# Kernel optimization log

Measured on AMD Instinct MI355X. Metric: run time of the kernel, lower is better.

Reference implementation:

```python
import jax, jax.numpy as jnp
import numpy as np

MAX_LEVEL = 3
FULL_LEN = 2 ** MAX_LEVEL  # wavelet_full_len for db1, mode='zero'


def _make_patterns():
    # Per-feature input to the DWT is [v, 0, ..., 0] (scalar zero-padded to 2**j).
    # Haar/db1 'zero' DWT of that signal is v times a fixed sparse pattern:
    # cA (len 1) = v*2^(-j/2); cD_k first element = v*2^(-k/2), rest zeros.
    pats = []
    for j in range(1, MAX_LEVEL + 1):
        vec = [2.0 ** (-j / 2.0)]                      # cA, length 1
        for k in range(1, j + 1):                      # cD_1 .. cD_j
            seg = np.zeros(2 ** (j - k))
            seg[0] = 2.0 ** (-k / 2.0)
            vec.extend(seg.tolist())
        full = np.zeros(FULL_LEN, dtype=np.float32)
        arr = np.asarray(vec, dtype=np.float32)
        full[: arr.shape[0]] = arr                     # F.pad to wavelet_full_len
        pats.append(full)
    return jnp.asarray(np.stack(pats))                 # (MAX_LEVEL, FULL_LEN)

_P = _make_patterns()


def _gumbel_hard(logits, gumb):
    # F.gumbel_softmax(logits, tau=1.0, hard=True), one sample per feature row.
    y = jax.nn.softmax(logits[None, :] + gumb, axis=-1)          # (feat, L)
    hard = jax.nn.one_hot(jnp.argmax(y, axis=-1), y.shape[-1], dtype=y.dtype)
    return jax.lax.stop_gradient(hard - y) + y                   # straight-through


def _wavelet_layer(x, logits, gumb, Wnl, bnl, Wwo, bwo):
    # Collapses the per-feature/per-level torch double loop:
    # xi_wave(level j) = v * (Wnl[f] . P[j]) + bnl[f]
    a = Wnl @ _P.T                       # (feat, levels)
    w = _gumbel_hard(logits, gumb)       # (feat, levels), one-hot rows
    coeff = jnp.sum(w * a, axis=-1)      # (feat,)
    agg = x * coeff + bnl                # (B, N, feat)
    return agg @ Wwo + bwo               # linear_out


def _mix(h, res_proj):
    diff = jnp.mean((h - res_proj) ** 2)
    th = jax.nn.sigmoid(diff)
    return th * h + (1.0 - th) * res_proj


def reference(x, adj, Wres, bres,
              Wg0, bg0, Wrg0, brg0, logits0, gumb0, Wnl0, bnl0, Wwo0, bwo0, Wrw0, brw0,
              Wg1, bg1, Wrg1, brg1, logits1, gumb1, Wnl1, bnl1, Wwo1, bwo1, Wrw1, brw1):
    res = x @ Wres + bres                                        # (B,N,Dout)
    # ---- layer 0 ----
    xg = jnp.einsum('ij,bjf->bif', adj, x) @ Wg0 + bg0           # 64->256: no residual add
    xg = _mix(xg, res @ Wrg0 + brg0)
    xw = _wavelet_layer(xg, logits0, gumb0, Wnl0, bnl0, Wwo0, bwo0) + xg  # 256==256: add
    xw = _mix(xw, res @ Wrw0 + brw0)
    # ---- layer 1 ----
    xg1 = jnp.einsum('ij,bjf->bif', adj, xw) @ Wg1 + bg1 + xw    # 256==256: add
    xg1 = _mix(xg1, res @ Wrg1 + brg1)
    xw1 = _wavelet_layer(xg1, logits1, gumb1, Wnl1, bnl1, Wwo1, bwo1)     # 256->64: no add
    xw1 = _mix(xw1, res @ Wrw1 + brw1)
    return xw1


def setup_inputs() -> dict:
    key = jax.random.key(0)
    ks = jax.random.split(key, 32)
    B, N, D_in, H, D_out = 128, 512, 64, 256, 64
    s = 0.05
    inp = {
        'x': jax.random.normal(ks[0], (B, N, D_in), jnp.float32),
        'adj': jax.random.uniform(ks[1], (N, N), jnp.float32) / N,
        'Wres': jax.random.normal(ks[2], (D_in, D_out), jnp.float32) * s,
        'bres': jax.random.normal(ks[3], (D_out,), jnp.float32) * s,
        'Wg0': jax.random.normal(ks[4], (D_in, H), jnp.float32) * s,
        'bg0': jax.random.normal(ks[5], (H,), jnp.float32) * s,
        'Wrg0': jax.random.normal(ks[6], (D_out, H), jnp.float32) * s,
        'brg0': jax.random.normal(ks[7], (H,), jnp.float32) * s,
        'logits0': jax.random.normal(ks[8], (3,), jnp.float32),
        'gumb0': jax.random.gumbel(ks[9], (H, 3), jnp.float32),
        'Wnl0': jax.random.normal(ks[10], (H, FULL_LEN), jnp.float32) * s,
        'bnl0': jax.random.normal(ks[11], (H,), jnp.float32) * s,
        'Wwo0': jax.random.normal(ks[12], (H, H), jnp.float32) * s,
        'bwo0': jax.random.normal(ks[13], (H,), jnp.float32) * s,
        'Wrw0': jax.random.normal(ks[14], (D_out, H), jnp.float32) * s,
        'brw0': jax.random.normal(ks[15], (H,), jnp.float32) * s,
        'Wg1': jax.random.normal(ks[16], (H, H), jnp.float32) * s,
        'bg1': jax.random.normal(ks[17], (H,), jnp.float32) * s,
        'Wrg1': jax.random.normal(ks[18], (D_out, H), jnp.float32) * s,
        'brg1': jax.random.normal(ks[19], (H,), jnp.float32) * s,
        'logits1': jax.random.normal(ks[20], (3,), jnp.float32),
        'gumb1': jax.random.gumbel(ks[21], (H, 3), jnp.float32),
        'Wnl1': jax.random.normal(ks[22], (H, FULL_LEN), jnp.float32) * s,
        'bnl1': jax.random.normal(ks[23], (H,), jnp.float32) * s,
        'Wwo1': jax.random.normal(ks[24], (H, D_out), jnp.float32) * s,
        'bwo1': jax.random.normal(ks[25], (D_out,), jnp.float32) * s,
        'Wrw1': jax.random.normal(ks[26], (D_out, D_out), jnp.float32) * s,
        'brw1': jax.random.normal(ks[27], (D_out,), jnp.float32) * s,
    }
    return inp
```

## Files before the change

kernel.cpp:

```cpp
#include <hip/hip_runtime.h>
#include <hip/hip_bf16.h>
#include <math.h>

#define BB   128
#define NN   512
#define DIN  64
#define HH   256
#define DOUT 64
#define BNR  (BB * NN)

typedef float  f32x4  __attribute__((ext_vector_type(4)));
typedef __bf16 bf16x8 __attribute__((ext_vector_type(8)));

#define GLP(p)  ((const __attribute__((address_space(1))) void*)(p))
#define LDSP(p) ((__attribute__((address_space(3))) void*)(p))

__constant__ float PAT[3][8] = {
    {0.70710678f, 0.70710678f, 0.f, 0.f, 0.f, 0.f, 0.f, 0.f},
    {0.5f,        0.70710678f, 0.f, 0.5f, 0.f, 0.f, 0.f, 0.f},
    {0.35355339f, 0.70710678f, 0.f, 0.f, 0.f, 0.5f, 0.f, 0.35355339f}
};

__device__ __forceinline__ unsigned short f2bfu(float x) {
    __hip_bfloat16 b = __float2bfloat16(x);
// ... 37 lines not shown
    __syncthreads();
    #pragma unroll
    for (int j = 0; j < FN; ++j) {
        int colb = (wn * (FN * 16) + j * 16 + lc) * 2;
        #pragma unroll
        for (int i = 0; i < FM; ++i) {
            int row0 = wm * (FM * 16) + i * 16 + lr4;
            #pragma unroll
            for (int r = 0; r < 4; ++r) {
                int row = row0 + r;
                *reinterpret_cast<unsigned short*>(
                    lds + row * (BN * 2) + (colb ^ (((row >> 2) & 3) << 5))) =
                    f2bfu(a[i][j][r]);
            }
        }
    }
    __syncthreads();
    const int TPR = BN / 8;
    const int RPP = 256 / TPR;
    #pragma unroll
    for (int p = 0; p < BM / RPP; ++p) {
        int row = p * RPP + tid / TPR;
        int cb = (tid % TPR) * 16;
        int pb = cb ^ (((row >> 2) & 3) << 5);
        uint4 v = *reinterpret_cast<const uint4*>(lds + row * (BN * 2) + pb);
        *reinterpret_cast<uint4*>(reinterpret_cast<char*>(C + base + (long)row * N) + cb) = v;
    }
}

template<int BM, int BN, int FM, int FN>
__device__ __forceinline__ void write_tileT(char* lds, f32x4 (&a)[FM][FN],
                                            __hip_bfloat16* __restrict__ CT,
                                            long baseT, int ldT, int tid)
{
    const int wave = tid >> 6;
    const int lane = tid & 63;
    const int wm = wave >> 1, wn = wave & 1;
    const int lc = lane & 15;
    const int lr4 = (lane >> 4) << 2;
    __syncthreads();
    #pragma unroll
    for (int j = 0; j < FN; ++j) {
        int c = wn * (FN * 16) + j * 16 + lc;
        int cbase = c * (BM * 2);
        int swz = ((c >> 2) & 3) << 5;
        #pragma unroll
        for (int i = 0; i < FM; ++i) {
            int m0 = wm * (FM * 16) + i * 16 + lr4;
            #pragma unroll
            for (int r = 0; r < 4; ++r) {
                int m = m0 + r;
                *reinterpret_cast<unsigned short*>(lds + cbase + ((m * 2) ^ swz)) =
                    f2bfu(a[i][j][r]);
            }
        }
    }
    __syncthreads();
    const int TPR = BM / 8;
    const int RPP = 256 / TPR;
    #pragma unroll
    for (int p = 0; p < BN / RPP; ++p) {
        int c = p * RPP + tid / TPR;
        int tb = (tid % TPR) * 16;
        int pb = tb ^ (((c >> 2) & 3) << 5);
        uint4 v = *reinterpret_cast<const uint4*>(lds + c * (BM * 2) + pb);
        *reinterpret_cast<uint4*>(reinterpret_cast<char*>(CT + baseT + (long)c * ldT) + tb) = v;
    }
}

template<int BM, int BN>
__device__ __forceinline__ void stage_tiles(const __hip_bfloat16* __restrict__ Ab,
                                            const __hip_bfloat16* __restrict__ Bb,
                                            char* AsB, char* BsB,
                                            int m0, int n0, int k0, int KA, int KB,
                                            int wave, int lane)
{
    const int NCH = (BM + BN) / 32;
    const int lr = lane >> 3;
    const int ls = lane & 7;
    #pragma unroll
    for (int cc = 0; cc < NCH; ++cc) {
        int c = wave * NCH + cc;
        const __hip_bfloat16* src;
        char* ldsb;
        if (c < BM / 8) {
            int r = c * 8 + lr;
            ldsb = AsB + c * 1024;
            src = Ab + ((long)(m0 + r) * KA + k0 + ((ls ^ (r & 7)) << 3));
        } else {
            int c2 = c - BM / 8;
            int r = c2 * 8 + lr;
            ldsb = BsB + c2 * 1024;
            src = Bb + ((long)(n0 + r) * KB + k0 + ((ls ^ (r & 7)) << 3));
        }
        __builtin_amdgcn_global_load_lds(GLP(src), LDSP(ldsb), 16, 0, 0);
    }
}

template<int BM, int BN, int FM, int FN>
__device__ __forceinline__ void mfma_tiles(char* AsB, char* BsB,
                                           f32x4 (&acc)[FM][FN], int wave, int lane)
{
    const int wm = wave >> 1, wn = wave & 1;
    #pragma unroll
    for (int ksl = 0; ksl < 2; ++ksl) {
        bf16x8 af[FM], bfr[FN];
        #pragma unroll
        for (int i = 0; i < FM; ++i) {
            int row = wm * (FM * 16) + i * 16 + (lane & 15);
            int off = (ksl * 64 + ((lane >> 4) << 4)) ^ ((row & 7) << 4);
            af[i] = *reinterpret_cast<const bf16x8*>(AsB + row * 128 + off);
        }
        #pragma unroll
        for (int j = 0; j < FN; ++j) {
            int row = wn * (FN * 16) + j * 16 + (lane & 15);
            int off = (ksl * 64 + ((lane >> 4) << 4)) ^ ((row & 7) << 4);
            bfr[j] = *reinterpret_cast<const bf16x8*>(BsB + row * 128 + off);
        }
        #pragma unroll
        for (int i = 0; i < FM; ++i)
            #pragma unroll
            for (int j = 0; j < FN; ++j)
                acc[i][j] = __builtin_amdgcn_mfma_f32_16x16x32_bf16(
                    af[i], bfr[j], acc[i][j], 0, 0, 0);
    }
}

template<int BM, int BN, int FM, int FN, int NS, int NA>
__device__ __forceinline__ void pipe_run(
    const __hip_bfloat16* const (&sA)[NS], const __hip_bfloat16* const (&sB)[NS],
    const int (&sK)[NS], const int (&sk0)[NS],
    char* buf0, char* buf1,
    f32x4 (&acc0)[FM][FN], f32x4 (&acc1)[FM][FN],
    int m0, int n0, int wave, int lane)
{
    constexpr int BOFF = BM * 128;
    stage_tiles<BM, BN>(sA[0], sB[0], buf0, buf0 + BOFF, m0, n0, sk0[0],
                        sK[0], sK[0], wave, lane);
    __syncthreads();
    #pragma unroll
    for (int t = 0; t < NS; ++t) {
        char* bc = (t & 1) ? buf1 : buf0;
        if (t + 1 < NS) {
            char* bn = (t & 1) ? buf0 : buf1;
            stage_tiles<BM, BN>(sA[t + 1], sB[t + 1], bn, bn + BOFF, m0, n0,
                                sk0[t + 1], sK[t + 1], sK[t + 1], wave, lane);
        }
        if (t < NA) mfma_tiles<BM, BN, FM, FN>(bc, bc + BOFF, acc0, wave, lane);
        else        mfma_tiles<BM, BN, FM, FN>(bc, bc + BOFF, acc1, wave, lane);
        __syncthreads();
    }
}

__global__ __launch_bounds__(256) void cvta_k(const float* __restrict__ adj,
                                              unsigned int* __restrict__ adjb,
                                              float* __restrict__ ars)
{
    int n = blockIdx.x;
    int t = threadIdx.x;
    float2 v = reinterpret_cast<const float2*>(adj)[n * 256 + t];
    adjb[n * 256 + t] = (unsigned int)f2bfu(v.x) | ((unsigned int)f2bfu(v.y) << 16);
    __shared__ float sm[256];
    sm[t] = v.x + v.y;
    __syncthreads();
    for (int o = 128; o > 0; o >>= 1) {
        if (t < o) sm[t] += sm[t + o];
        __syncthreads();
    }
    if (t == 0) ars[n] = sm[0];
}

__global__ __launch_bounds__(256) void cvtx_k(const float* __restrict__ in,
                                              unsigned short* __restrict__ rm,
                                              unsigned short* __restrict__ tr)
{
    __shared__ float t[64][65];
    const long base = (long)blockIdx.z * NN * DIN;
    const int r0 = blockIdx.y * 64;
    const int tr4 = threadIdx.x >> 6;
    const int tc  = threadIdx.x & 63;
    #pragma unroll
    for (int i = 0; i < 16; ++i) {
        int r = i * 4 + tr4;
        float v = in[base + (long)(r0 + r) * DIN + tc];
        t[r][tc] = v;
        rm[base + (long)(r0 + r) * DIN + tc] = f2bfu(v);
    }
    __syncthreads();
    #pragma unroll
    for (int i = 0; i < 16; ++i) {
        int d = i * 4 + tr4;
        tr[base + (long)d * NN + r0 + tc] = f2bfu(t[tc][d]);
    }
}

__device__ __forceinline__ void tcvt_body(const float* __restrict__ in,
                                          unsigned short* __restrict__ out,
                                          const float* __restrict__ cs, float us,
                                          int R, int C, int r0, int c0)
{
    __shared__ float t[64][65];
    int tr = threadIdx.x >> 6;
    int tc = threadIdx.x & 63;
    #pragma unroll
    for (int i = 0; i < 16; ++i) {
        int r = i * 4 + tr;
        t[r][tc] = in[(long)(r0 + r) * C + c0 + tc];
    }
    __syncthreads();
    float sc = (cs ? cs[r0 + tc] : 1.0f) * us;
    #pragma unroll
    for (int i = 0; i < 16; ++i) {
        int r = i * 4 + tr;
        out[(long)(c0 + r) * R + r0 + tc] = f2bfu(t[tc][r] * sc);
    }
}

struct WTArgs {
    const float* src[8];
    unsigned short* dst[8];
    const float* cs[8];
    float sgn[8];
    int R[8], C[8];
};
__global__ __launch_bounds__(256) void tcvt_w_k(WTArgs a)
{
    int wgt = blockIdx.y;
    int R = a.R[wgt], C = a.C[wgt];
    int tilesX = C >> 6;
    int tiles = (R >> 6) * tilesX;
    int t = blockIdx.x;
    if (t >= tiles) return;
    tcvt_body(a.src[wgt], a.dst[wgt], a.cs[wgt], a.sgn[wgt], R, C,
              (t / tilesX) * 64, (t % tilesX) * 64);
}

__global__ void coeff2_k(const float* __restrict__ logits0, const float* __restrict__ gumb0,
                         const float* __restrict__ Wnl0, float* __restrict__ c0,
                         const float* __restrict__ logits1, const float* __restrict__ gumb1,
                         const float* __restrict__ Wnl1, float* __restrict__ c1)
{
    const float* lg = blockIdx.x ? logits1 : logits0;
    const float* gb = blockIdx.x ? gumb1 : gumb0;
    const float* Wn = blockIdx.x ? Wnl1 : Wnl0;
    float* cc = blockIdx.x ? c1 : c0;
    int f = threadIdx.x;
    float l0 = lg[0] + gb[f * 3 + 0];
    float l1 = lg[1] + gb[f * 3 + 1];
    float l2 = lg[2] + gb[f * 3 + 2];
    int bl = 0;
    float bv = l0;
    if (l1 > bv) { bv = l1; bl = 1; }
    if (l2 > bv) { bv = l2; bl = 2; }
    float s = 0.f;
    #pragma unroll
    for (int t = 0; t < 8; ++t) s += Wn[f * 8 + t] * PAT[bl][t];
    cc[f] = s;
}

struct FVArgs {
    const float* W[6];
    const float* c[6];
    const float* v[6];
    const float* base[6];
    float* out[6];
    int K[6], N[6];
};
__global__ __launch_bounds__(256) void foldvec_k(FVArgs a)
{
    int cs = blockIdx.y;
    int n = blockIdx.x;
    if (n >= a.N[cs]) return;
    int k = threadIdx.x;
    float s = 0.f;
    if (k < a.K[cs]) {
        float cc = a.c[cs] ? a.c[cs][k] : 1.0f;
        s = a.v[cs][k] * cc * a.W[cs][(long)k * a.N[cs] + n];
    }
    __shared__ float sm[256];
    sm[threadIdx.x] = s;
    __syncthreads();
    for (int o = 128; o > 0; o >>= 1) {
        if (threadIdx.x < o) sm[threadIdx.x] += sm[threadIdx.x + o];
        __syncthreads();
    }
    if (threadIdx.x == 0)
        a.out[cs][n] = (a.base[cs] ? a.base[cs][n] : 0.f) + sm[0];
}

struct WFArgs {
    const float* Wsrc[4];
    const float* Wbig[4];
    const float* c[4];
    int incl[4], N[4];
    unsigned short* dst[4];
};
__global__ __launch_bounds__(256) void wfold_k(WFArgs a)
{
    int cs = blockIdx.y;
    int m = blockIdx.x;
    __shared__ float ws[256];
    const float* c = a.c[cs];
    ws[threadIdx.x] = a.Wsrc[cs][m * 256 + threadIdx.x] * (c ? c[threadIdx.x] : 1.0f);
    __syncthreads();
    int n = threadIdx.x;
    int N = a.N[cs];
    if (n >= N) return;
    float s = a.incl[cs] ? a.Wsrc[cs][m * 256 + n] : 0.f;
    const float* Wb = a.Wbig[cs];
    #pragma unroll 8
    for (int k = 0; k < 256; ++k)
        s += ws[k] * Wb[(long)k * N + n];
    a.dst[cs][n * 64 + m] = f2bfu(s);
}

__global__ __launch_bounds__(256) void sc0_k(
    const float* __restrict__ partial, int np, float inv_n,
    unsigned short* __restrict__ Wa,
    unsigned short* __restrict__ Wb,
    const float* __restrict__ bg0p, const float* __restrict__ brg0p,
    const float* __restrict__ crow0, float* __restrict__ cv0)
{
    __shared__ float red[256];
    float th = block_th(partial, np, inv_n, red, threadIdx.x);
    float om = 1.f - th;
    int g = blockIdx.x * 256 + threadIdx.x;
    Wa[g] = f2bfu(th * bf2f(Wa[g]));
    Wb[g] = f2bfu(om * bf2f(Wb[g]));
    if (g < 256) cv0[g] = th * bg0p[g] + om * brg0p[g] + crow0[g];
}

__global__ __launch_bounds__(256) void sc1_k(
    const float* __restrict__ partial, int np, float inv_n,
    unsigned short* __restrict__ Wg1T,
    const unsigned short* __restrict__ Wrw0T, const unsigned short* __restrict__ Wrg0pT,
    unsigned short* __restrict__ WcombT,
    unsigned short* __restrict__ Wg0pT,
    unsigned short* __restrict__ WrwWg1T,
    const float* __restrict__ bg1, const float* __restrict__ brw0,
    const float* __restrict__ cv0, const float* __restrict__ bw1v,
    float* __restrict__ bv1g, float* __restrict__ bw1s)
{
    __shared__ float red[256];
    float th = block_th(partial, np, inv_n, red, threadIdx.x);
    float om = 1.f - th;
    int g = blockIdx.x * 256 + threadIdx.x;
    Wg1T[g] = f2bfu(th * bf2f(Wg1T[g]));
    if (g < 16384) {
        WcombT[g]  = f2bfu(th * bf2f(Wrg0pT[g]) + om * bf2f(Wrw0T[g]));
        Wg0pT[g]   = f2bfu(th * bf2f(Wg0pT[g]));
        WrwWg1T[g] = f2bfu(om * bf2f(WrwWg1T[g]));
    }
    if (g < 256) {
        bv1g[g] = bg1[g] + om * brw0[g] + th * cv0[g];
        bw1s[g] = om * bw1v[g];
    }
}

__global__ __launch_bounds__(256) void sc2_k(
    const float* __restrict__ partial, int np, float inv_n,
    unsigned short* __restrict__ Wc1T,
    unsigned short* __restrict__ Wrgc1T,
    const float* __restrict__ brgc1, const float* __restrict__ crow1,
    float* __restrict__ cv2)
{
    __shared__ float red[256];
    float th = block_th(partial, np, inv_n, red, threadIdx.x);
    float om = 1.f - th;
    int g = blockIdx.x * 256 + threadIdx.x;
    Wc1T[g] = f2bfu(th * bf2f(Wc1T[g]));
    if (g < 4096) Wrgc1T[g] = f2bfu(om * bf2f(Wrgc1T[g]));
    if (g < 64) cv2[g] = om * brgc1[g] + crow1[g];
}

template<int BM, int BN, int FM, int FN>
__global__ __launch_bounds__(256) void gemm_res_k(
    const __hip_bfloat16* __restrict__ A, const __hip_bfloat16* __restrict__ Bt,
    const float* __restrict__ bias,
    __hip_bfloat16* __restrict__ Cb, __hip_bfloat16* __restrict__ CbT,
    int M, int N, int K)
{
    __shared__ __attribute__((aligned(128))) char lds[(BM + BN) * 128];
    char* AsB = lds;
    char* BsB = lds + BM * 128;

    const int m0 = blockIdx.y * BM;
    const int tid  = threadIdx.x;
    const int wave = tid >> 6;
    const int lane = tid & 63;
    const int wn = wave & 1;

    f32x4 acc[FM][FN];
    #pragma unroll
    for (int i = 0; i < FM; ++i)
        #pragma unroll
        for (int j = 0; j < FN; ++j)
            acc[i][j] = (f32x4){0.f, 0.f, 0.f, 0.f};

    for (int k0 = 0; k0 < K; k0 += 64) {
        stage_tiles<BM, BN>(A, Bt, AsB, BsB, m0, 0, k0, K, K, wave, lane);
        __syncthreads();
        mfma_tiles<BM, BN, FM, FN>(AsB, BsB, acc, wave, lane);
        __syncthreads();
    }

    const int lc = lane & 15;
    #pragma unroll
    for (int j = 0; j < FN; ++j) {
        float bv = bias[wn * (FN * 16) + j * 16 + lc];
        #pragma unroll
        for (int i = 0; i < FM; ++i)
            #pragma unroll
            for (int r = 0; r < 4; ++r)
                acc[i][j][r] += bv;
    }
    write_tile<BM, BN, FM, FN>(lds, acc, Cb, (long)m0 * N, N, tid);
    long baseT = (long)(m0 / NN) * ((long)N * NN) + (m0 % NN);
    write_tileT<BM, BN, FM, FN>(lds, acc, CbT, baseT, NN, tid);
}

template<int BM, int BN, int FM, int FN, int GX, int NB, int NS>
__global__ __launch_bounds__(256) void gemm_bt_swz_k(
    const __hip_bfloat16* __restrict__ A, const __hip_bfloat16* __restrict__ Bt,
    __hip_bfloat16* __restrict__ Cb,
    int M, int N, int K, long sA, long sB, long sC)
{
    __shared__ __attribute__((aligned(128))) char lds[2 * (BM + BN) * 128];

    const int d   = blockIdx.x;
    const int xcd = d & 7;
    const int q   = d >> 3;
    const int t   = q % NB;
    const int bz  = xcd + ((q / NB) << 3);
    const int n0  = (t % GX) * BN;
    const int m0  = (t / GX) * BM;

    const __hip_bfloat16* Ab = A + (long)bz * sA;
    const __hip_bfloat16* Bb = Bt + (long)bz * sB;

    const int tid  = threadIdx.x;
    const int wave = tid >> 6;
    const int lane = tid & 63;

    f32x4 acc[FM][FN];
    #pragma unroll
    for (int i = 0; i < FM; ++i)
        #pragma unroll
        for (int j = 0; j < FN; ++j)
            acc[i][j] = (f32x4){0.f, 0.f, 0.f, 0.f};

    const __hip_bfloat16* pA[NS];
    const __hip_bfloat16* pB[NS];
    int pK[NS], pk0[NS];
    #pragma unroll
    for (int s = 0; s < NS; ++s) { pA[s] = Ab; pB[s] = Bb; pK[s] = K; pk0[s] = s * 64; }

    pipe_run<BM, BN, FM, FN, NS, NS>(pA, pB, pK, pk0,
                                     lds, lds + (BM + BN) * 128,
                                     acc, acc, m0, n0, wave, lane);

    write_tile<BM, BN, FM, FN>(lds, acc, Cb, (long)bz * sC + (long)m0 * N + n0, N, tid);
}

template<int BM, int BN, int FM, int FN>
__global__ __launch_bounds__(256) void dual1_k(
    const __hip_bfloat16* __restrict__ A0, const __hip_bfloat16* __restrict__ B0, int K0,
    const __hip_bfloat16* __restrict__ A1, const __hip_bfloat16* __restrict__ B1, int K1,
    const float* __restrict__ b1, const float* __restrict__ b2,
    float* __restrict__ partial, int M, int N)
{
    __shared__ __attribute__((aligned(128))) char lds[2 * (BM + BN) * 128];

    const int d   = blockIdx.x;
    const int q   = d >> 3;
    const int nx  = q & 1;
    const int my  = (d & 7) + ((q >> 1) << 3);
    const int m0  = my * BM;
    const int n0  = nx * BN;

    const int tid  = threadIdx.x;
    const int wave = tid >> 6;
    const int lane = tid & 63;
    const int wn = wave & 1;

    f32x4 acc[FM][FN];
    #pragma unroll
    for (int i = 0; i < FM; ++i)
        #pragma unroll
        for (int j = 0; j < FN; ++j)
            acc[i][j] = (f32x4){0.f, 0.f, 0.f, 0.f};

    const __hip_bfloat16* pA[2] = {A0, A1};
    const __hip_bfloat16* pB[2] = {B0, B1};
    int pK[2] = {K0, K1};
    int pk0[2] = {0, 0};
    pipe_run<BM, BN, FM, FN, 2, 2>(pA, pB, pK, pk0,
                                   lds, lds + (BM + BN) * 128,
                                   acc, acc, m0, n0, wave, lane);

    const int lc = lane & 15;
    float dsum = 0.f;
    #pragma unroll
    for (int j = 0; j < FN; ++j) {
        int col = n0 + wn * (FN * 16) + j * 16 + lc;
        float bd = b1[col] - b2[col];
        #pragma unroll
        for (int i = 0; i < FM; ++i)
            #pragma unroll
            for (int r = 0; r < 4; ++r) {
                float dd = acc[i][j][r] + bd;
                dsum += dd * dd;
            }
    }

    float* red = (float*)lds;
    red[tid] = dsum;
    __syncthreads();
    for (int o = 128; o > 0; o >>= 1) {
        if (tid < o) red[tid] += red[tid + o];
        __syncthreads();
    }
    if (tid == 0) partial[my * 2 + nx] = red[0];
}

template<int BM, int BN, int FM, int FN>
__global__ __launch_bounds__(256) void wave2T_k(
    const __hip_bfloat16* __restrict__ A0, const __hip_bfloat16* __restrict__ B0, int K0,
    const __hip_bfloat16* __restrict__ A1, const __hip_bfloat16* __restrict__ B1, int K1,
    const __hip_bfloat16* __restrict__ A2, const __hip_bfloat16* __restrict__ B2, int K2,
    const float* __restrict__ cv, const float* __restrict__ b2v,
    __hip_bfloat16* __restrict__ C1T, float* __restrict__ partial_out, int M, int N)
{
    __shared__ __attribute__((aligned(128))) char lds[2 * (BM + BN) * 128];

    const int d   = blockIdx.x;
    const int q   = d >> 3;
    const int nx  = q & 1;
    const int my  = (d & 7) + ((q >> 1) << 3);
    const int m0  = my * BM;
    const int n0  = nx * BN;

    const int tid  = threadIdx.x;
    const int wave = tid >> 6;
    const int lane = tid & 63;
    const int wn = wave & 1;

    f32x4 acc0[FM][FN], acc1[FM][FN];
    #pragma unroll
    for (int i = 0; i < FM; ++i)
        #pragma unroll
        for (int j = 0; j < FN; ++j) {
            acc0[i][j] = (f32x4){0.f, 0.f, 0.f, 0.f};
            acc1[i][j] = (f32x4){0.f, 0.f, 0.f, 0.f};
        }

    const __hip_bfloat16* pA[3] = {A0, A1, A2};
    const __hip_bfloat16* pB[3] = {B0, B1, B2};
    int pK[3] = {K0, K1, K2};
    int pk0[3] = {0, 0, 0};
    pipe_run<BM, BN, FM, FN, 3, 2>(pA, pB, pK, pk0,
                                   lds, lds + (BM + BN) * 128,
                                   acc0, acc1, m0, n0, wave, lane);

    const int lc = lane & 15;
    float dsum = 0.f;
    #pragma unroll
    for (int j = 0; j < FN; ++j) {
        int col = n0 + wn * (FN * 16) + j * 16 + lc;
        float c1 = cv[col];
        float c2 = b2v[col];
        #pragma unroll
// ... 132 lines not shown
    const __hip_bfloat16* pA[6] = {A0, A0, A0, A0, A1, A2};
    const __hip_bfloat16* pB[6] = {B0, B0, B0, B0, B1, B2};
    int pK[6]  = {K0, K0, K0, K0, K1, K2};
    int pk0[6] = {0, 64, 128, 192, 0, 0};
    pipe_run<BM, BN, FM, FN, 6, 5>(pA, pB, pK, pk0,
                                   lds, lds + (BM + BN) * 128,
                                   acc0, acc1, m0, n0, wave, lane);

    const int lc = lane & 15;
    float dsum = 0.f;
    #pragma unroll
    for (int j = 0; j < FN; ++j) {
        int col = n0 + wn * (FN * 16) + j * 16 + lc;
        float c1 = cv[col];
        float c2 = b2v[col];
        #pragma unroll
        for (int i = 0; i < FM; ++i)
            #pragma unroll
            for (int r = 0; r < 4; ++r) {
                float v1 = acc0[i][j][r] + c1;
                float v2 = acc1[i][j][r] + c2;
                acc0[i][j][r] = v1;
                acc1[i][j][r] = v2;
                float dd = v1 - v2;
                dsum += dd * dd;
            }
    }

    float* red = (float*)lds;
    red[tid] = dsum;
    __syncthreads();
    for (int o = 128; o > 0; o >>= 1) {
        if (tid < o) red[tid] += red[tid + o];
        __syncthreads();
    }
    if (tid == 0) partial_out[pidx] = red[0];

    write_tile<BM, BN, FM, FN>(lds, acc0, C1, (long)m0 * N + n0, N, tid);
    write_tile<BM, BN, FM, FN>(lds, acc1, C2, (long)m0 * N + n0, N, tid);
}

__global__ __launch_bounds__(256) void mixfinal_k(
    const unsigned short* __restrict__ h, const unsigned short* __restrict__ r,
    const float* __restrict__ partial_in, int np_in, float inv_in,
    float* __restrict__ out, long n4)
{
    __shared__ float sm[256];
    const float th = block_th(partial_in, np_in, inv_in, sm, (int)threadIdx.x);
    const float om = 1.f - th;
    long gid = (long)blockIdx.x * 256 + threadIdx.x;
    long stride = (long)gridDim.x * 256;
    for (long i = gid; i < n4; i += stride) {
        ushort4 hv = reinterpret_cast<const ushort4*>(h)[i];
        ushort4 rv = reinterpret_cast<const ushort4*>(r)[i];
        float4 o;
        o.x = th * bf2f(hv.x) + om * bf2f(rv.x);
        o.y = th * bf2f(hv.y) + om * bf2f(rv.y);
        o.z = th * bf2f(hv.z) + om * bf2f(rv.z);
        o.w = th * bf2f(hv.w) + om * bf2f(rv.w);
        reinterpret_cast<float4*>(out)[i] = o;
    }
}

extern "C" void kernel_launch(void* const* d_in, const int* in_sizes, int n_in,
                              void* d_out, int out_size, void* d_ws, size_t ws_size,
                              hipStream_t stream)
{
    const float* x       = (const float*)d_in[0];
    const float* adj     = (const float*)d_in[1];
    const float* Wres    = (const float*)d_in[2];
    const float* bres    = (const float*)d_in[3];
    const float* Wg0     = (const float*)d_in[4];
    const float* bg0     = (const float*)d_in[5];
    const float* Wrg0    = (const float*)d_in[6];
    const float* brg0    = (const float*)d_in[7];
    const float* logits0 = (const float*)d_in[8];
    const float* gumb0   = (const float*)d_in[9];
    const float* Wnl0    = (const float*)d_in[10];
    const float* bnl0    = (const float*)d_in[11];
    const float* Wwo0    = (const float*)d_in[12];
    const float* bwo0    = (const float*)d_in[13];
    const float* Wrw0    = (const float*)d_in[14];
    const float* brw0    = (const float*)d_in[15];
    const float* Wg1     = (const float*)d_in[16];
    const float* bg1     = (const float*)d_in[17];
    const float* Wrg1    = (const float*)d_in[18];
    const float* brg1    = (const float*)d_in[19];
    const float* logits1 = (const float*)d_in[20];
    const float* gumb1   = (const float*)d_in[21];
    const float* Wnl1    = (const float*)d_in[22];
    const float* bnl1    = (const float*)d_in[23];
    const float* Wwo1    = (const float*)d_in[24];
    const float* bwo1    = (const float*)d_in[25];
    const float* Wrw1    = (const float*)d_in[26];
    const float* brw1    = (const float*)d_in[27];

    float* out = (float*)d_out;

    char* w = (char*)d_ws;
    auto alloc = [&](long bytes) { char* p = w; w += (bytes + 255) & ~255L; return p; };
    const long SLOT = (long)BNR * HH * 2;
    char* pool = alloc(5 * SLOT);
    __hip_bfloat16* Rbf  = (__hip_bfloat16*)alloc((long)BNR * DOUT * 2);
    __hip_bfloat16* adjb = (__hip_bfloat16*)alloc((long)NN * NN * 2);
    __hip_bfloat16* WT   = (__hip_bfloat16*)alloc(225280L * 2);
    float* partial0 = (float*)alloc(2048 * 4);
    float* partial1 = (float*)alloc(2048 * 4);
    float* partial2 = (float*)alloc(2048 * 4);
    float* partial3 = (float*)alloc(2048 * 4);
    float* c0      = (float*)alloc(256 * 4);
    float* c1      = (float*)alloc(256 * 4);
    float* bg0p    = (float*)alloc(256 * 4);
    float* brg0p   = (float*)alloc(256 * 4);
    float* crow0   = (float*)alloc(256 * 4);
    float* brgc1   = (float*)alloc(64 * 4);
    float* crow1   = (float*)alloc(64 * 4);
    float* cv0     = (float*)alloc(256 * 4);
    float* bv1g    = (float*)alloc(256 * 4);
    float* cv2     = (float*)alloc(64 * 4);
    float* ars     = (float*)alloc(512 * 4);
    float* bw1v    = (float*)alloc(256 * 4);
    float* bw1s    = (float*)alloc(256 * 4);

    auto S = [&](int i) { return pool + (long)i * SLOT; };
    __hip_bfloat16* xwrT = (__hip_bfloat16*)S(0);
    __hip_bfloat16* orw  = (__hip_bfloat16*)S(1);
    __hip_bfloat16* rw1  = (__hip_bfloat16*)(S(1) + (long)BNR * DOUT * 2);
    __hip_bfloat16* Radj = (__hip_bfloat16*)(S(1) + 2L * BNR * DOUT * 2);
    __hip_bfloat16* xg1  = (__hip_bfloat16*)S(2);
    __hip_bfloat16* T1x  = (__hip_bfloat16*)S(3);
    __hip_bfloat16* xbf  = (__hip_bfloat16*)S(4);
    __hip_bfloat16* xT   = (__hip_bfloat16*)(S(4) + (long)BNR * DIN * 2);
    __hip_bfloat16* T0   = (__hip_bfloat16*)(S(4) + 2L * BNR * DIN * 2);
    __hip_bfloat16* RbfT = (__hip_bfloat16*)(S(4) + 3L * BNR * DIN * 2);

    __hip_bfloat16* WresT   = WT;
    __hip_bfloat16* Wg0T    = WT + 4096;
    __hip_bfloat16* Wrg0T   = WT + 20480;
    __hip_bfloat16* Wrw0T   = WT + 36864;
    __hip_bfloat16* Wg1T    = WT + 53248;
    __hip_bfloat16* Wrg1T   = WT + 118784;
    __hip_bfloat16* Wc1T    = WT + 135168;
    __hip_bfloat16* Wrw1T   = WT + 151552;
    __hip_bfloat16* Wg0pT   = WT + 155648;
    __hip_bfloat16* Wrg0pT  = WT + 172032;
    __hip_bfloat16* Wrgc1T  = WT + 188416;
    __hip_bfloat16* WcombT  = WT + 192512;
    __hip_bfloat16* WrwWg1T = WT + 208896;

    const dim3 blk(256);
    const float invH = 1.0f / ((float)BNR * HH);
    const float invD = 1.0f / ((float)BNR * DOUT);

    hipLaunchKernelGGL(coeff2_k, dim3(2), dim3(256), 0, stream,
                       logits0, gumb0, Wnl0, c0, logits1, gumb1, Wnl1, c1);
    hipLaunchKernelGGL(cvta_k, dim3(NN), blk, 0, stream, adj, (unsigned int*)adjb, ars);
    hipLaunchKernelGGL(cvtx_k, dim3(1, 8, BB), blk, 0, stream, x,
                       (unsigned short*)xbf, (unsigned short*)xT);

    WTArgs wa;
    wa.src[0] = Wres; wa.dst[0] = (unsigned short*)WresT; wa.cs[0] = nullptr; wa.sgn[0] = 1.f;  wa.R[0] = 64;  wa.C[0] = 64;
    wa.src[1] = Wg0;  wa.dst[1] = (unsigned short*)Wg0T;  wa.cs[1] = nullptr; wa.sgn[1] = 1.f;  wa.R[1] = 64;  wa.C[1] = 256;
    wa.src[2] = Wrg0; wa.dst[2] = (unsigned short*)Wrg0T; wa.cs[2] = nullptr; wa.sgn[2] = -1.f; wa.R[2] = 64;  wa.C[2] = 256;
    wa.src[3] = Wrw0; wa.dst[3] = (unsigned short*)Wrw0T; wa.cs[3] = nullptr; wa.sgn[3] = 1.f;  wa.R[3] = 64;  wa.C[3] = 256;
    wa.src[4] = Wg1;  wa.dst[4] = (unsigned short*)Wg1T;  wa.cs[4] = nullptr; wa.sgn[4] = 1.f;  wa.R[4] = 256; wa.C[4] = 256;
    wa.src[5] = Wrg1; wa.dst[5] = (unsigned short*)Wrg1T; wa.cs[5] = nullptr; wa.sgn[5] = 1.f;  wa.R[5] = 64;  wa.C[5] = 256;
    wa.src[6] = Wwo1; wa.dst[6] = (unsigned short*)Wc1T;  wa.cs[6] = c1;      wa.sgn[6] = 1.f;  wa.R[6] = 256; wa.C[6] = 64;
    wa.src[7] = Wrw1; wa.dst[7] = (unsigned short*)Wrw1T; wa.cs[7] = nullptr; wa.sgn[7] = 1.f;  wa.R[7] = 64;  wa.C[7] = 64;
    hipLaunchKernelGGL(tcvt_w_k, dim3(16, 8), blk, 0, stream, wa);

    WFArgs wf;
    wf.Wsrc[0] = Wg0;  wf.Wbig[0] = Wwo0; wf.c[0] = c0;      wf.incl[0] = 1; wf.N[0] = 256;
    wf.dst[0] = (unsigned short*)Wg0pT;
    wf.Wsrc[1] = Wrg0; wf.Wbig[1] = Wwo0; wf.c[1] = c0;      wf.incl[1] = 1; wf.N[1] = 256;
    wf.dst[1] = (unsigned short*)Wrg0pT;
    wf.Wsrc[2] = Wrg1; wf.Wbig[2] = Wwo1; wf.c[2] = c1;      wf.incl[2] = 0; wf.N[2] = 64;
    wf.dst[2] = (unsigned short*)Wrgc1T;
    wf.Wsrc[3] = Wrw0; wf.Wbig[3] = Wg1;  wf.c[3] = nullptr; wf.incl[3] = 0; wf.N[3] = 256;
    wf.dst[3] = (unsigned short*)WrwWg1T;
    hipLaunchKernelGGL(wfold_k, dim3(64, 4), blk, 0, stream, wf);

    FVArgs fv;
    fv.W[0] = Wwo0; fv.c[0] = c0;      fv.v[0] = bg0;  fv.base[0] = bg0;     fv.out[0] = bg0p;  fv.K[0] = 256; fv.N[0] = 256;
    fv.W[1] = Wwo0; fv.c[1] = c0;      fv.v[1] = brg0; fv.base[1] = brg0;    fv.out[1] = brg0p; fv.K[1] = 256; fv.N[1] = 256;
    fv.W[2] = Wwo0; fv.c[2] = nullptr; fv.v[2] = bnl0; fv.base[2] = bwo0;    fv.out[2] = crow0; fv.K[2] = 256; fv.N[2] = 256;
    fv.W[3] = Wwo1; fv.c[3] = c1;      fv.v[3] = brg1; fv.base[3] = nullptr; fv.out[3] = brgc1; fv.K[3] = 256; fv.N[3] = 64;
    fv.W[4] = Wwo1; fv.c[4] = nullptr; fv.v[4] = bnl1; fv.base[4] = bwo1;    fv.out[4] = crow1; fv.K[4] = 256; fv.N[4] = 64;
    fv.W[5] = Wg1;  fv.c[5] = nullptr; fv.v[5] = brw0; fv.base[5] = nullptr; fv.out[5] = bw1v;  fv.K[5] = 256; fv.N[5] = 256;
    hipLaunchKernelGGL(foldvec_k, dim3(256, 6), blk, 0, stream, fv);

    hipLaunchKernelGGL((gemm_res_k<128, 64, 4, 2>), dim3(1, BNR / 128, 1), blk, 0, stream,
                       xbf, WresT, bres, Rbf, RbfT, BNR, DOUT, DIN);

    hipLaunchKernelGGL((gemm_bt_swz_k<128, 64, 4, 2, 1, 4, 8>), dim3(BB * 4), blk, 0, stream,
                       adjb, xT, T0, NN, DIN, NN, 0, (long)DIN * NN, (long)NN * DIN);

    hipLaunchKernelGGL((gemm_bt_swz_k<128, 64, 4, 2, 1, 4, 8>), dim3(BB * 4), blk, 0, stream,
                       adjb, RbfT, Radj, NN, DOUT, NN, 0, (long)DOUT * NN, (long)NN * DOUT);

    hipLaunchKernelGGL((dual1_k<64, 128, 2, 4>), dim3(2 * BNR / 64), blk, 0, stream,
                       T0, Wg0T, DIN, Rbf, Wrg0T, DOUT, bg0, brg0, partial0, BNR, HH);

    hipLaunchKernelGGL(sc0_k, dim3(64), blk, 0, stream, partial0, 2048, invH,
                       (unsigned short*)Wg0pT, (unsigned short*)Wrg0pT,
                       bg0p, brg0p, crow0, cv0);

    hipLaunchKernelGGL((wave2T_k<64, 128, 2, 4>), dim3(2 * BNR / 64), blk, 0, stream,
                       T0, Wg0pT, DIN, Rbf, Wrg0pT, DOUT, Rbf, Wrw0T, DOUT,
                       cv0, brw0, xwrT, partial1, BNR, HH);

    hipLaunchKernelGGL(sc1_k, dim3(256), blk, 0, stream, partial1, 2048, invH,
                       (unsigned short*)Wg1T,
                       (const unsigned short*)Wrw0T, (const unsigned short*)Wrg0pT,
                       (unsigned short*)WcombT,
                       (unsigned short*)Wg0pT,
                       (unsigned short*)WrwWg1T,
                       bg1, brw0, cv0, bw1v, bv1g, bw1s);

    hipLaunchKernelGGL((gemm_bt_swz_k<128, 64, 4, 2, 4, 16, 8>), dim3(BB * 16), blk, 0, stream,
                       adjb, xwrT, T1x, NN, HH, NN, 0, (long)HH * NN, (long)NN * HH);

    hipLaunchKernelGGL((gmix5_k<64, 128, 2, 4>), dim3(2 * BNR / 64), blk, 0, stream,
                       T1x, Wg1T, HH,
                       Radj, WrwWg1T, DOUT,
                       T0, Wg0pT, DIN,
                       Rbf, WcombT, DOUT,
                       Rbf, Wrg1T, DOUT,
                       bv1g, brg1, ars, bw1s, xg1, partial2, BNR, HH);

    hipLaunchKernelGGL(sc2_k, dim3(64), blk, 0, stream, partial2, 2048, invH,
                       (unsigned short*)Wc1T, (unsigned short*)Wrgc1T,
                       brgc1, crow1, cv2);

    hipLaunchKernelGGL((wave2_k<64, 64, 2, 2>), dim3(1, BNR / 64), blk, 0, stream,
                       xg1, Wc1T, HH, Rbf, Wrgc1T, DOUT, Rbf, Wrw1T, DIN,
                       cv2, brw1, orw, rw1, partial3, BNR, DOUT);

    hipLaunchKernelGGL(mixfinal_k, dim3(2048), blk, 0, stream,
                       (const unsigned short*)orw, (const unsigned short*)rw1,
                       partial3, 1024, invD, out, (long)BNR * DOUT / 4);
}
```

Measured before the change: 178.2 us.

## Merge prep kernels and fuse adj GEMMs sharing the A tile

Collapses the coefficient, adjacency-convert and x-convert kernels into one launch, and the weight transpose, weight-fold and bias-fold kernels into another, cutting the number of small kernel launches. It also replaces the two batched adj@x and adj@Rbf GEMMs with one kernel that stages each adj tile once and runs MFMAs against both B operands, reusing the A tile and halving its loads. The trade-offs are more LDS per block and higher register pressure in the fused GEMM. The foldvec work is now serialized over six cases inside each block.

```diff
diff --git a/kernel.cpp b/kernel.cpp
--- a/kernel.cpp
+++ b/kernel.cpp
@@ -213,48 +213,6 @@
     }
 }
 
-__global__ __launch_bounds__(256) void cvta_k(const float* __restrict__ adj,
-                                              unsigned int* __restrict__ adjb,
-                                              float* __restrict__ ars)
-{
-    int n = blockIdx.x;
-    int t = threadIdx.x;
-    float2 v = reinterpret_cast<const float2*>(adj)[n * 256 + t];
-    adjb[n * 256 + t] = (unsigned int)f2bfu(v.x) | ((unsigned int)f2bfu(v.y) << 16);
-    __shared__ float sm[256];
-    sm[t] = v.x + v.y;
-    __syncthreads();
-    for (int o = 128; o > 0; o >>= 1) {
-        if (t < o) sm[t] += sm[t + o];
-        __syncthreads();
-    }
-    if (t == 0) ars[n] = sm[0];
-}
-
-__global__ __launch_bounds__(256) void cvtx_k(const float* __restrict__ in,
-                                              unsigned short* __restrict__ rm,
-                                              unsigned short* __restrict__ tr)
-{
-    __shared__ float t[64][65];
-    const long base = (long)blockIdx.z * NN * DIN;
-    const int r0 = blockIdx.y * 64;
-    const int tr4 = threadIdx.x >> 6;
-    const int tc  = threadIdx.x & 63;
-    #pragma unroll
-    for (int i = 0; i < 16; ++i) {
-        int r = i * 4 + tr4;
-        float v = in[base + (long)(r0 + r) * DIN + tc];
-        t[r][tc] = v;
-        rm[base + (long)(r0 + r) * DIN + tc] = f2bfu(v);
-    }
-    __syncthreads();
-    #pragma unroll
-    for (int i = 0; i < 16; ++i) {
-        int d = i * 4 + tr4;
-        tr[base + (long)d * NN + r0 + tc] = f2bfu(t[tc][d]);
-    }
-}
-
 __device__ __forceinline__ void tcvt_body(const float* __restrict__ in,
                                           unsigned short* __restrict__ out,
                                           const float* __restrict__ cs, float us,
@@ -284,41 +242,13 @@
     float sgn[8];
     int R[8], C[8];
 };
-__global__ __launch_bounds__(256) void tcvt_w_k(WTArgs a)
-{
-    int wgt = blockIdx.y;
-    int R = a.R[wgt], C = a.C[wgt];
-    int tilesX = C >> 6;
-    int tiles = (R >> 6) * tilesX;
-    int t = blockIdx.x;
-    if (t >= tiles) return;
-    tcvt_body(a.src[wgt], a.dst[wgt], a.cs[wgt], a.sgn[wgt], R, C,
-              (t / tilesX) * 64, (t % tilesX) * 64);
-}
-
-__global__ void coeff2_k(const float* __restrict__ logits0, const float* __restrict__ gumb0,
-                         const float* __restrict__ Wnl0, float* __restrict__ c0,
-                         const float* __restrict__ logits1, const float* __restrict__ gumb1,
-                         const float* __restrict__ Wnl1, float* __restrict__ c1)
-{
-    const float* lg = blockIdx.x ? logits1 : logits0;
-    const float* gb = blockIdx.x ? gumb1 : gumb0;
-    const float* Wn = blockIdx.x ? Wnl1 : Wnl0;
-    float* cc = blockIdx.x ? c1 : c0;
-    int f = threadIdx.x;
-    float l0 = lg[0] + gb[f * 3 + 0];
-    float l1 = lg[1] + gb[f * 3 + 1];
-    float l2 = lg[2] + gb[f * 3 + 2];
-    int bl = 0;
-    float bv = l0;
-    if (l1 > bv) { bv = l1; bl = 1; }
-    if (l2 > bv) { bv = l2; bl = 2; }
-    float s = 0.f;
-    #pragma unroll
-    for (int t = 0; t < 8; ++t) s += Wn[f * 8 + t] * PAT[bl][t];
-    cc[f] = s;
-}
-
+struct WFArgs {
+    const float* Wsrc[4];
+    const float* Wbig[4];
+    const float* c[4];
+    int incl[4], N[4];
+    unsigned short* dst[4];
+};
 struct FVArgs {
     const float* W[6];
     const float* c[6];
@@ -327,58 +257,127 @@
     float* out[6];
     int K[6], N[6];
 };
-__global__ __launch_bounds__(256) void foldvec_k(FVArgs a)
-{
-    int cs = blockIdx.y;
-    int n = blockIdx.x;
-    if (n >= a.N[cs]) return;
-    int k = threadIdx.x;
-    float s = 0.f;
-    if (k < a.K[cs]) {
-        float cc = a.c[cs] ? a.c[cs][k] : 1.0f;
-        s = a.v[cs][k] * cc * a.W[cs][(long)k * a.N[cs] + n];
-    }
-    __shared__ float sm[256];
-    sm[threadIdx.x] = s;
-    __syncthreads();
-    for (int o = 128; o > 0; o >>= 1) {
-        if (threadIdx.x < o) sm[threadIdx.x] += sm[threadIdx.x + o];
-        __syncthreads();
-    }
-    if (threadIdx.x == 0)
-        a.out[cs][n] = (a.base[cs] ? a.base[cs][n] : 0.f) + sm[0];
-}
-
-struct WFArgs {
-    const float* Wsrc[4];
-    const float* Wbig[4];
-    const float* c[4];
-    int incl[4], N[4];
-    unsigned short* dst[4];
-};
-__global__ __launch_bounds__(256) void wfold_k(WFArgs a)
-{
-    int cs = blockIdx.y;
-    int m = blockIdx.x;
-    __shared__ float ws[256];
-    const float* c = a.c[cs];
-    ws[threadIdx.x] = a.Wsrc[cs][m * 256 + threadIdx.x] * (c ? c[threadIdx.x] : 1.0f);
-    __syncthreads();
-    int n = threadIdx.x;
-    int N = a.N[cs];
-    if (n >= N) return;
-    float s = a.incl[cs] ? a.Wsrc[cs][m * 256 + n] : 0.f;
-    const float* Wb = a.Wbig[cs];
-    #pragma unroll 8
-    for (int k = 0; k < 256; ++k)
-        s += ws[k] * Wb[(long)k * N + n];
-    a.dst[cs][n * 64 + m] = f2bfu(s);
+
+__global__ __launch_bounds__(256) void prep1_k(
+    const float* __restrict__ logits0, const float* __restrict__ gumb0,
+    const float* __restrict__ Wnl0, float* __restrict__ c0,
+    const float* __restrict__ logits1, const float* __restrict__ gumb1,
+    const float* __restrict__ Wnl1, float* __restrict__ c1,
+    const float* __restrict__ adj, unsigned int* __restrict__ adjb,
+    float* __restrict__ ars,
+    const float* __restrict__ x, unsigned short* __restrict__ xbf,
+    unsigned short* __restrict__ xT)
+{
+    __shared__ float shm[64 * 65];
+    const int b = blockIdx.x;
+    const int t = threadIdx.x;
+    if (b < 2) {
+        const float* lg = b ? logits1 : logits0;
+        const float* gb = b ? gumb1 : gumb0;
+        const float* Wn = b ? Wnl1 : Wnl0;
+        float* cc = b ? c1 : c0;
+        float l0 = lg[0] + gb[t * 3 + 0];
+        float l1 = lg[1] + gb[t * 3 + 1];
+        float l2 = lg[2] + gb[t * 3 + 2];
+        int bl = 0;
+        float bv = l0;
+        if (l1 > bv) { bv = l1; bl = 1; }
+        if (l2 > bv) { bv = l2; bl = 2; }
+        float s = 0.f;
+        #pragma unroll
+        for (int q = 0; q < 8; ++q) s += Wn[t * 8 + q] * PAT[bl][q];
+        cc[t] = s;
+    } else if (b < 2 + NN) {
+        int n = b - 2;
+        float2 v = reinterpret_cast<const float2*>(adj)[n * 256 + t];
+        adjb[n * 256 + t] = (unsigned int)f2bfu(v.x) | ((unsigned int)f2bfu(v.y) << 16);
+        shm[t] = v.x + v.y;
+        __syncthreads();
+        for (int o = 128; o > 0; o >>= 1) {
+            if (t < o) shm[t] += shm[t + o];
+            __syncthreads();
+        }
+        if (t == 0) ars[n] = shm[0];
+    } else {
+        int tt = b - 2 - NN;
+        int bz = tt >> 3;
+        int r0 = (tt & 7) * 64;
+        float (*tl)[65] = (float(*)[65])shm;
+        const long base = (long)bz * NN * DIN;
+        const int tr4 = t >> 6;
+        const int tc  = t & 63;
+        #pragma unroll
+        for (int i = 0; i < 16; ++i) {
+            int r = i * 4 + tr4;
+            float v = x[base + (long)(r0 + r) * DIN + tc];
+            tl[r][tc] = v;
+            xbf[base + (long)(r0 + r) * DIN + tc] = f2bfu(v);
+        }
+        __syncthreads();
+        #pragma unroll
+        for (int i = 0; i < 16; ++i) {
+            int d = i * 4 + tr4;
+            xT[base + (long)d * NN + r0 + tc] = f2bfu(tl[tc][d]);
+        }
+    }
+}
+
+__global__ __launch_bounds__(256) void prep2_k(WTArgs wa, WFArgs wf, FVArgs fv)
+{
+    __shared__ float aux[256];
+    if (blockIdx.y == 0) {
+        int xg = blockIdx.x;
+        int wgt = xg >> 4;
+        if (wgt >= 8) return;
+        int t = xg & 15;
+        int R = wa.R[wgt], C = wa.C[wgt];
+        int tilesX = C >> 6;
+        int tiles = (R >> 6) * tilesX;
+        if (t >= tiles) return;
+        tcvt_body(wa.src[wgt], wa.dst[wgt], wa.cs[wgt], wa.sgn[wgt], R, C,
+                  (t / tilesX) * 64, (t % tilesX) * 64);
+    } else if (blockIdx.y == 1) {
+        int xg = blockIdx.x;
+        int cs = xg >> 6;
+        int m = xg & 63;
+        const float* c = wf.c[cs];
+        aux[threadIdx.x] = wf.Wsrc[cs][m * 256 + threadIdx.x] * (c ? c[threadIdx.x] : 1.0f);
+        __syncthreads();
+        int n = threadIdx.x;
+        int N = wf.N[cs];
+        if (n >= N) return;
+        float s = wf.incl[cs] ? wf.Wsrc[cs][m * 256 + n] : 0.f;
+        const float* Wb = wf.Wbig[cs];
+        #pragma unroll 8
+        for (int k = 0; k < 256; ++k)
+            s += aux[k] * Wb[(long)k * N + n];
+        wf.dst[cs][n * 64 + m] = f2bfu(s);
+    } else {
+        int n = blockIdx.x;
+        for (int cs = 0; cs < 6; ++cs) {
+            __syncthreads();
+            if (n >= fv.N[cs]) continue;
+            int k = threadIdx.x;
+            float s = 0.f;
+            if (k < fv.K[cs]) {
+                float cc = fv.c[cs] ? fv.c[cs][k] : 1.0f;
+                s = fv.v[cs][k] * cc * fv.W[cs][(long)k * fv.N[cs] + n];
+            }
+            aux[threadIdx.x] = s;
+            __syncthreads();
+            for (int o = 128; o > 0; o >>= 1) {
+                if (threadIdx.x < o) aux[threadIdx.x] += aux[threadIdx.x + o];
+                __syncthreads();
+            }
+            if (threadIdx.x == 0)
+                fv.out[cs][n] = (fv.base[cs] ? fv.base[cs][n] : 0.f) + aux[0];
+        }
+    }
 }
 
 __global__ __launch_bounds__(256) void sc0_k(
     const float* __restrict__ partial, int np, float inv_n,
-    unsigned short* __restrict__ Wa,
-    unsigned short* __restrict__ Wb,
+    unsigned short* __restrict__ Wa, unsigned short* __restrict__ Wb,
     const float* __restrict__ bg0p, const float* __restrict__ brg0p,
     const float* __restrict__ crow0, float* __restrict__ cv0)
 {
@@ -420,8 +419,7 @@
 
 __global__ __launch_bounds__(256) void sc2_k(
     const float* __restrict__ partial, int np, float inv_n,
-    unsigned short* __restrict__ Wc1T,
-    unsigned short* __restrict__ Wrgc1T,
+    unsigned short* __restrict__ Wc1T, unsigned short* __restrict__ Wrgc1T,
     const float* __restrict__ brgc1, const float* __restrict__ crow1,
     float* __restrict__ cv2)
 {
@@ -478,6 +476,83 @@
     write_tile<BM, BN, FM, FN>(lds, acc, Cb, (long)m0 * N, N, tid);
     long baseT = (long)(m0 / NN) * ((long)N * NN) + (m0 % NN);
     write_tileT<BM, BN, FM, FN>(lds, acc, CbT, baseT, NN, tid);
+}
+
+__global__ __launch_bounds__(256) void t0radj_k(
+    const __hip_bfloat16* __restrict__ adjb,
+    const __hip_bfloat16* __restrict__ xT,
+    const __hip_bfloat16* __restrict__ RbfT,
+    __hip_bfloat16* __restrict__ T0,
+    __hip_bfloat16* __restrict__ Radj)
+{
+    constexpr int BM = 128, BN = 64;
+    constexpr int ABYTES = BM * 128;
+    constexpr int BBYTES = BN * 128;
+    constexpr int BUF = ABYTES + 2 * BBYTES;
+    __shared__ __attribute__((aligned(128))) char lds[2 * BUF];
+
+    const int d   = blockIdx.x;
+    const int xcd = d & 7;
+    const int q   = d >> 3;
+    const int t   = q & 3;
+    const int bz  = xcd + ((q >> 2) << 3);
+    const int m0  = t * BM;
+
+    const __hip_bfloat16* B1 = xT + (long)bz * (64L * NN);
+    const __hip_bfloat16* B2 = RbfT + (long)bz * (64L * NN);
+
+    const int tid  = threadIdx.x;
+    const int wave = tid >> 6;
+    const int lane = tid & 63;
+    const int lr = lane >> 3;
+    const int ls = lane & 7;
+
+    f32x4 accA[4][2], accB[4][2];
+    #pragma unroll
+    for (int i = 0; i < 4; ++i)
+        #pragma unroll
+        for (int j = 0; j < 2; ++j) {
+            accA[i][j] = (f32x4){0.f, 0.f, 0.f, 0.f};
+            accB[i][j] = (f32x4){0.f, 0.f, 0.f, 0.f};
+        }
+
+    auto stage2 = [&](char* buf, int k0) {
+        #pragma unroll
+        for (int cc = 0; cc < 8; ++cc) {
+            int c = wave * 8 + cc;
+            const __hip_bfloat16* src;
+            char* ldsb;
+            if (c < 16) {
+                int r = c * 8 + lr;
+                ldsb = buf + c * 1024;
+                src = adjb + ((long)(m0 + r) * NN + k0 + ((ls ^ (r & 7)) << 3));
+            } else if (c < 24) {
+                int r = (c - 16) * 8 + lr;
+                ldsb = buf + ABYTES + (c - 16) * 1024;
+                src = B1 + ((long)r * NN + k0 + ((ls ^ (r & 7)) << 3));
+            } else {
+                int r = (c - 24) * 8 + lr;
+                ldsb = buf + ABYTES + BBYTES + (c - 24) * 1024;
+                src = B2 + ((long)r * NN + k0 + ((ls ^ (r & 7)) << 3));
+            }
+            __builtin_amdgcn_global_load_lds(GLP(src), LDSP(ldsb), 16, 0, 0);
+        }
+    };
+
+    stage2(lds, 0);
+    __syncthreads();
+    #pragma unroll
+    for (int s = 0; s < 8; ++s) {
+        char* bc = lds + (s & 1) * BUF;
+        if (s + 1 < 8) stage2(lds + ((s + 1) & 1) * BUF, (s + 1) * 64);
+        mfma_tiles<BM, BN, 4, 2>(bc, bc + ABYTES, accA, wave, lane);
+        mfma_tiles<BM, BN, 4, 2>(bc, bc + ABYTES + BBYTES, accB, wave, lane);
+        __syncthreads();
+    }
+
+    long base = (long)bz * ((long)NN * BN) + (long)m0 * BN;
+    write_tile<BM, BN, 4, 2>(lds, accA, T0, base, BN, tid);
+    write_tile<BM, BN, 4, 2>(lds, accB, Radj, base, BN, tid);
 }
 
 template<int BM, int BN, int FM, int FN, int GX, int NB, int NS>
@@ -916,11 +991,10 @@
     const float invH = 1.0f / ((float)BNR * HH);
     const float invD = 1.0f / ((float)BNR * DOUT);
 
-    hipLaunchKernelGGL(coeff2_k, dim3(2), dim3(256), 0, stream,
-                       logits0, gumb0, Wnl0, c0, logits1, gumb1, Wnl1, c1);
-    hipLaunchKernelGGL(cvta_k, dim3(NN), blk, 0, stream, adj, (unsigned int*)adjb, ars);
-    hipLaunchKernelGGL(cvtx_k, dim3(1, 8, BB), blk, 0, stream, x,
-                       (unsigned short*)xbf, (unsigned short*)xT);
+    hipLaunchKernelGGL(prep1_k, dim3(2 + NN + 8 * BB), blk, 0, stream,
+                       logits0, gumb0, Wnl0, c0, logits1, gumb1, Wnl1, c1,
+                       adj, (unsigned int*)adjb, ars,
+                       x, (unsigned short*)xbf, (unsigned short*)xT);
 
     WTArgs wa;
     wa.src[0] = Wres; wa.dst[0] = (unsigned short*)WresT; wa.cs[0] = nullptr; wa.sgn[0] = 1.f;  wa.R[0] = 64;  wa.C[0] = 64;
@@ -931,7 +1005,6 @@
     wa.src[5] = Wrg1; wa.dst[5] = (unsigned short*)Wrg1T; wa.cs[5] = nullptr; wa.sgn[5] = 1.f;  wa.R[5] = 64;  wa.C[5] = 256;
     wa.src[6] = Wwo1; wa.dst[6] = (unsigned short*)Wc1T;  wa.cs[6] = c1;      wa.sgn[6] = 1.f;  wa.R[6] = 256; wa.C[6] = 64;
     wa.src[7] = Wrw1; wa.dst[7] = (unsigned short*)Wrw1T; wa.cs[7] = nullptr; wa.sgn[7] = 1.f;  wa.R[7] = 64;  wa.C[7] = 64;
-    hipLaunchKernelGGL(tcvt_w_k, dim3(16, 8), blk, 0, stream, wa);
 
     WFArgs wf;
     wf.Wsrc[0] = Wg0;  wf.Wbig[0] = Wwo0; wf.c[0] = c0;      wf.incl[0] = 1; wf.N[0] = 256;
@@ -942,7 +1015,6 @@
     wf.dst[2] = (unsigned short*)Wrgc1T;
     wf.Wsrc[3] = Wrw0; wf.Wbig[3] = Wg1;  wf.c[3] = nullptr; wf.incl[3] = 0; wf.N[3] = 256;
     wf.dst[3] = (unsigned short*)WrwWg1T;
-    hipLaunchKernelGGL(wfold_k, dim3(64, 4), blk, 0, stream, wf);
 
     FVArgs fv;
     fv.W[0] = Wwo0; fv.c[0] = c0;      fv.v[0] = bg0;  fv.base[0] = bg0;     fv.out[0] = bg0p;  fv.K[0] = 256; fv.N[0] = 256;
@@ -951,16 +1023,13 @@
     fv.W[3] = Wwo1; fv.c[3] = c1;      fv.v[3] = brg1; fv.base[3] = nullptr; fv.out[3] = brgc1; fv.K[3] = 256; fv.N[3] = 64;
     fv.W[4] = Wwo1; fv.c[4] = nullptr; fv.v[4] = bnl1; fv.base[4] = bwo1;    fv.out[4] = crow1; fv.K[4] = 256; fv.N[4] = 64;
     fv.W[5] = Wg1;  fv.c[5] = nullptr; fv.v[5] = brw0; fv.base[5] = nullptr; fv.out[5] = bw1v;  fv.K[5] = 256; fv.N[5] = 256;
-    hipLaunchKernelGGL(foldvec_k, dim3(256, 6), blk, 0, stream, fv);
+    hipLaunchKernelGGL(prep2_k, dim3(256, 3), blk, 0, stream, wa, wf, fv);
 
     hipLaunchKernelGGL((gemm_res_k<128, 64, 4, 2>), dim3(1, BNR / 128, 1), blk, 0, stream,
                        xbf, WresT, bres, Rbf, RbfT, BNR, DOUT, DIN);
 
-    hipLaunchKernelGGL((gemm_bt_swz_k<128, 64, 4, 2, 1, 4, 8>), dim3(BB * 4), blk, 0, stream,
-                       adjb, xT, T0, NN, DIN, NN, 0, (long)DIN * NN, (long)NN * DIN);
-
-    hipLaunchKernelGGL((gemm_bt_swz_k<128, 64, 4, 2, 1, 4, 8>), dim3(BB * 4), blk, 0, stream,
-                       adjb, RbfT, Radj, NN, DOUT, NN, 0, (long)DOUT * NN, (long)NN * DOUT);
+    hipLaunchKernelGGL(t0radj_k, dim3(BB * 4), blk, 0, stream,
+                       adjb, xT, RbfT, T0, Radj);
 
     hipLaunchKernelGGL((dual1_k<64, 128, 2, 4>), dim3(2 * BNR / 64), blk, 0, stream,
                        T0, Wg0T, DIN, Rbf, Wrg0T, DOUT, bg0, brg0, partial0, BNR, HH);
```

Result: faster. 161.4 us (-9.4%).
